# Optimization experiments

Hardware: AMD Instinct MI355X
Metric: run time of the kernel (lower is better)

## Reference

```python
import jax, jax.numpy as jnp
import numpy as np

N_QUBITS = 4
N_LAYERS = 2
DIM = 2 ** N_QUBITS  # 16
BATCH, INPUT_SIZE, HIDDEN_SIZE = 65536, 128, 512

# PennyLane default.qubit convention: wire 0 is the most significant bit.
def _cnot_perm(c, t, n=N_QUBITS):
    idx = np.arange(2 ** n)
    cbit = (idx >> (n - 1 - c)) & 1
    return np.where(cbit == 1, idx ^ (1 << (n - 1 - t)), idx)

# ring of CNOTs: control j -> target (j+1)%n
CNOT_PERMS = [jnp.asarray(_cnot_perm(j, (j + 1) % N_QUBITS)) for j in range(N_QUBITS)]
_idx = np.arange(DIM)
Z_SIGNS = jnp.asarray(np.stack([1.0 - 2.0 * ((_idx >> (N_QUBITS - 1 - j)) & 1) for j in range(N_QUBITS)], axis=1).astype(np.float32))  # [16, 4]


def _rx(t):
    c = jnp.cos(t / 2).astype(jnp.complex64)
    s = (-1j * jnp.sin(t / 2)).astype(jnp.complex64)
    return jnp.stack([jnp.stack([c, s]), jnp.stack([s, c])])


def _ry(t):
    c = jnp.cos(t / 2).astype(jnp.complex64)
    s = jnp.sin(t / 2).astype(jnp.complex64)
    return jnp.stack([jnp.stack([c, -s]), jnp.stack([s, c])])


def _rz(t):
    e = jnp.exp(-0.5j * t.astype(jnp.complex64))
    z = jnp.zeros((), jnp.complex64)
    return jnp.stack([jnp.stack([e, z]), jnp.stack([z, jnp.conj(e)])])


def _apply_1q(state, gate, j, n=N_QUBITS):
    # state: [B, 2^n] complex; gate: [2,2] (shared) or [B,2,2] (per-sample)
    B = state.shape[0]
    st = state.reshape(B, 2 ** j, 2, 2 ** (n - 1 - j))
    if gate.ndim == 2:
        st = jnp.einsum('ij,bajc->baic', gate, st)
    else:
        st = jnp.einsum('bij,bajc->baic', gate, st)
    return st.reshape(B, 2 ** n)


def _qlayer(angles, qweights):
    # Batched 4-qubit state-vector sim of the PennyLane circuit.
    # angles: [B, 4] float32 (RY embedding); qweights: [2, 4, 3]
    B = angles.shape[0]
    state = jnp.zeros((B, DIM), jnp.complex64).at[:, 0].set(1.0)
    c = jnp.cos(angles / 2).astype(jnp.complex64)
    s = jnp.sin(angles / 2).astype(jnp.complex64)
    for j in range(N_QUBITS):
        gate = jnp.stack([jnp.stack([c[:, j], -s[:, j]], -1), jnp.stack([s[:, j], c[:, j]], -1)], -2)  # [B,2,2]
        state = _apply_1q(state, gate, j)
    for l in range(N_LAYERS):
        for j in range(N_QUBITS):
            state = state[:, CNOT_PERMS[j]]
        for j in range(N_QUBITS):
            state = _apply_1q(state, _rx(qweights[l, j, 0]), j)
            state = _apply_1q(state, _ry(qweights[l, j, 1]), j)
            state = _apply_1q(state, _rz(qweights[l, j, 2]), j)
    probs = state.real ** 2 + state.imag ** 2  # [B, 16]
    return probs @ Z_SIGNS  # [B, 4] expval(PauliZ_j)


def _gate(combined, pw, pb, qw, lw, lb):
    ang = combined @ pw.T + pb  # [B, 4]
    # torch original runs the circuit on detached numpy and wraps the result in
    # torch.tensor -> no gradient flows through the quantum layer.
    q = jax.lax.stop_gradient(_qlayer(ang, qw))
    return q @ lw.T + lb  # [B, hidden]


GATES = ('forget', 'input', 'output', 'cell')


def setup_inputs() -> dict:
    key = jax.random.key(0)
    ks = jax.random.split(key, 3 + 3 * len(GATES))
    inp = {
        'x': jax.random.normal(ks[0], (BATCH, INPUT_SIZE), jnp.float32),
        'h_prev': jax.random.normal(ks[1], (BATCH, HIDDEN_SIZE), jnp.float32),
        'c_prev': jax.random.normal(ks[2], (BATCH, HIDDEN_SIZE), jnp.float32),
    }
    for i, g in enumerate(GATES):
        k0, k1, k2 = ks[3 + 3 * i], ks[4 + 3 * i], ks[5 + 3 * i]
        inp[g + '_proj_w'] = jax.random.normal(k0, (N_QUBITS, INPUT_SIZE + HIDDEN_SIZE), jnp.float32) * 0.02
        inp[g + '_proj_b'] = jnp.zeros((N_QUBITS,), jnp.float32)
        inp[g + '_qw'] = jax.random.normal(k1, (N_LAYERS, N_QUBITS, 3), jnp.float32) * 0.1
        inp[g + '_lin_w'] = jax.random.normal(k2, (HIDDEN_SIZE, N_QUBITS), jnp.float32) * 0.1
        inp[g + '_lin_b'] = jnp.zeros((HIDDEN_SIZE,), jnp.float32)
    return inp


def reference(x, h_prev, c_prev,
              forget_proj_w, forget_proj_b, forget_qw, forget_lin_w, forget_lin_b,
              input_proj_w, input_proj_b, input_qw, input_lin_w, input_lin_b,
              output_proj_w, output_proj_b, output_qw, output_lin_w, output_lin_b,
              cell_proj_w, cell_proj_b, cell_qw, cell_lin_w, cell_lin_b):
    combined = jnp.concatenate([x, h_prev], axis=1)  # [B, in+hid]
    f = jax.nn.sigmoid(_gate(combined, forget_proj_w, forget_proj_b, forget_qw, forget_lin_w, forget_lin_b))
    i = jax.nn.sigmoid(_gate(combined, input_proj_w, input_proj_b, input_qw, input_lin_w, input_lin_b))
    o = jax.nn.sigmoid(_gate(combined, output_proj_w, output_proj_b, output_qw, output_lin_w, output_lin_b))
    g = jnp.tanh(_gate(combined, cell_proj_w, cell_proj_b, cell_qw, cell_lin_w, cell_lin_b))
    c_next = f * c_prev + i * g
    h_next = o * jnp.tanh(c_next)
    return (h_next, c_next)
```

## Files before the change

### kernel.cpp

```cpp
#include <hip/hip_runtime.h>
#include <math.h>

#define BATCHN 65536
#define INPUTN 128
#define HIDDENN 512
#define CATN 640
#define ROWS_LSTM 32
#define LDSROW 144

typedef float f2v __attribute__((ext_vector_type(2)));
typedef float f4v __attribute__((ext_vector_type(4)));
typedef short s8v __attribute__((ext_vector_type(8)));

__device__ __forceinline__ unsigned short f2bf_rne(float f) {
  unsigned u = __float_as_uint(f);
  u += 0x7fffu + ((u >> 16) & 1u);
  return (unsigned short)(u >> 16);
}

__device__ __forceinline__ uint2 pack_bf16x4(float4 a) {
  uint2 u;
  asm("v_cvt_pk_bf16_f32 %0, %1, %2" : "=v"(u.x) : "v"(a.x), "v"(a.y));
  asm("v_cvt_pk_bf16_f32 %0, %1, %2" : "=v"(u.y) : "v"(a.z), "v"(a.w));
  return u;
}

__global__ void k_prologue(const float* __restrict__ qwF, const float* __restrict__ qwI,
                           const float* __restrict__ qwO, const float* __restrict__ qwC,
                           const float* __restrict__ pwF, const float* __restrict__ pwI,
                           const float* __restrict__ pwO, const float* __restrict__ pwC,
                           float2* __restrict__ U, unsigned short* __restrict__ Bfrag) {
  const int t = threadIdx.x;
  if (t < 64) {
    int g = t >> 4, col = t & 15;
    const float* qw = (g == 0) ? qwF : (g == 1) ? qwI : (g == 2) ? qwO : qwC;

    float sr[16], si[16];
#pragma unroll
    for (int i = 0; i < 16; i++) { sr[i] = (i == col) ? 1.f : 0.f; si[i] = 0.f; }

#pragma unroll
    for (int l = 0; l < 2; l++) {
#pragma unroll
      for (int j = 0; j < 4; j++) {
        const int bc = 8 >> j;
        const int bt = 8 >> ((j + 1) & 3);
        float tr[16], ti[16];
#pragma unroll
        for (int i = 0; i < 16; i++) {
          int src = (i & bc) ? (i ^ bt) : i;
          tr[i] = sr[src]; ti[i] = si[src];
        }
#pragma unroll
        for (int i = 0; i < 16; i++) { sr[i] = tr[i]; si[i] = ti[i]; }
      }
#pragma unroll
      for (int j = 0; j < 4; j++) {
        const int bit = 8 >> j;
        const float thx = qw[(l * 4 + j) * 3 + 0] * 0.5f;
        const float thy = qw[(l * 4 + j) * 3 + 1] * 0.5f;
        const float thz = qw[(l * 4 + j) * 3 + 2] * 0.5f;
        float c, s;
        c = cosf(thx); s = sinf(thx);
#pragma unroll
        for (int i = 0; i < 16; i++) if (!(i & bit)) {
          const int k2 = i | bit;
          const float ar = sr[i], ai = si[i], br = sr[k2], bi = si[k2];
          sr[i]  = c * ar + s * bi;  si[i]  = c * ai - s * br;
          sr[k2] = c * br + s * ai;  si[k2] = c * bi - s * ar;
        }
        c = cosf(thy); s = sinf(thy);
#pragma unroll
        for (int i = 0; i < 16; i++) if (!(i & bit)) {
          const int k2 = i | bit;
          const float ar = sr[i], ai = si[i], br = sr[k2], bi = si[k2];
          sr[i]  = c * ar - s * br;  si[i]  = c * ai - s * bi;
          sr[k2] = s * ar + c * br;  si[k2] = s * ai + c * bi;
        }
        c = cosf(thz); s = sinf(thz);
#pragma unroll
        for (int i = 0; i < 16; i++) if (!(i & bit)) {
          const int k2 = i | bit;
          const float ar = sr[i], ai = si[i], br = sr[k2], bi = si[k2];
          sr[i]  = c * ar + s * ai;  si[i]  = c * ai - s * ar;
          sr[k2] = c * br - s * bi;  si[k2] = c * bi + s * br;
        }
      }
    }
#pragma unroll
    for (int m = 0; m < 16; m++)
      U[(g * 16 + m) * 16 + col] = make_float2(sr[m], si[m]);
  }

  for (int e = t; e < 20 * 64; e += 256) {
    const int s = e >> 6, l = e & 63;
    const int n = l & 15, kb = l >> 4;
    const int gate = n >> 2, orow = n & 3;
    const float* pw = (gate == 0) ? pwF : (gate == 1) ? pwI : (gate == 2) ? pwO : pwC;
    const int k0 = s * 32 + kb * 8;
    unsigned short* dst = Bfrag + (size_t)e * 8;
#pragma unroll
    for (int j = 0; j < 8; ++j) dst[j] = f2bf_rne(pw[orow * CATN + k0 + j]);
  }
}

__global__ __launch_bounds__(256) void k_proj_q(
    const float* __restrict__ x, const float* __restrict__ hprev,
    const float* __restrict__ pbF, const float* __restrict__ pbI,
    const float* __restrict__ pbO, const float* __restrict__ pbC,
    const float2* __restrict__ U, const unsigned short* __restrict__ Bfrag,
    float* __restrict__ qv) {
  __shared__ char ldsA[2][64 * LDSROW];
  __shared__ float angL[64 * 17];
  const int tid = threadIdx.x;
  const int lane = tid & 63;
  const int wv = tid >> 6;
  const int m0 = wv * 16;
  const size_t rb = (size_t)blockIdx.x * 64;

  const int c4 = tid & 15;
  const int r0 = tid >> 4;

  {
    float4 v[4];
#pragma unroll
    for (int p = 0; p < 4; ++p)
      v[p] = *(const float4*)(x + (rb + r0 + p * 16) * INPUTN + c4 * 4);
#pragma unroll
    for (int p = 0; p < 4; ++p)
      *(uint2*)&ldsA[0][(r0 + p * 16) * LDSROW + c4 * 8] = pack_bf16x4(v[p]);
  }
  __syncthreads();

  f4v acc = {0.f, 0.f, 0.f, 0.f};
  const int aoff = (m0 + (lane & 15)) * LDSROW + (lane >> 4) * 16;

#pragma unroll 1
  for (int T = 0; T < 10; ++T) {
    float4 nv0, nv1, nv2, nv3;
    const bool more = (T + 1 < 10);
    if (more) {
      const int gk = (T + 1) * 64 + c4 * 4;
      const float* base = (gk < INPUTN) ? (x + gk) : (hprev + (gk - INPUTN));
      const size_t stride = (gk < INPUTN) ? INPUTN : HIDDENN;
      nv0 = *(const float4*)(base + (rb + r0 +  0) * stride);
      nv1 = *(const float4*)(base + (rb + r0 + 16) * stride);
      nv2 = *(const float4*)(base + (rb + r0 + 32) * stride);
      nv3 = *(const float4*)(base + (rb + r0 + 48) * stride);
    }
    const s8v b0 = *(const s8v*)(Bfrag + ((size_t)(T * 2 + 0) * 64 + lane) * 8);
    const s8v b1 = *(const s8v*)(Bfrag + ((size_t)(T * 2 + 1) * 64 + lane) * 8);
    const char* ab = &ldsA[T & 1][aoff];
    const s8v a0 = *(const s8v*)(ab);
    const s8v a1 = *(const s8v*)(ab + 64);
    acc = __builtin_amdgcn_mfma_f32_16x16x32_bf16(a0, b0, acc, 0, 0, 0);
    acc = __builtin_amdgcn_mfma_f32_16x16x32_bf16(a1, b1, acc, 0, 0, 0);

    if (more) {
      char* dst = ldsA[(T + 1) & 1];
      *(uint2*)&dst[(r0 +  0) * LDSROW + c4 * 8] = pack_bf16x4(nv0);
      *(uint2*)&dst[(r0 + 16) * LDSROW + c4 * 8] = pack_bf16x4(nv1);
      *(uint2*)&dst[(r0 + 32) * LDSROW + c4 * 8] = pack_bf16x4(nv2);
      *(uint2*)&dst[(r0 + 48) * LDSROW + c4 * 8] = pack_bf16x4(nv3);
      __syncthreads();
    }
  }

#pragma unroll
  for (int r = 0; r < 4; ++r)
    angL[(m0 + (lane >> 4) * 4 + r) * 17 + (lane & 15)] = acc[r];
  __syncthreads();

  const int row = tid & 63;
  const float* pbg = (wv == 0) ? pbF : (wv == 1) ? pbI : (wv == 2) ? pbO : pbC;
  float ang[4];
#pragma unroll
  for (int j = 0; j < 4; ++j) ang[j] = angL[row * 17 + wv * 4 + j] + pbg[j];

  float cs[4], sn[4];
#pragma unroll
  for (int j = 0; j < 4; j++) __sincosf(ang[j] * 0.5f, &sn[j], &cs[j]);
  float psi[16];
#pragma unroll
  for (int c16 = 0; c16 < 16; c16++) {
    float p = ((c16 & 8) ? sn[0] : cs[0]);
    p *= ((c16 & 4) ? sn[1] : cs[1]);
    p *= ((c16 & 2) ? sn[2] : cs[2]);
    p *= ((c16 & 1) ? sn[3] : cs[3]);
    psi[c16] = p;
  }
  const float2* Ug = U + wv * 256;
  float q0 = 0.f, q1 = 0.f, q2 = 0.f, q3 = 0.f;
#pragma unroll
  for (int m = 0; m < 16; m++) {
    float ssr = 0.f, ssi = 0.f;
#pragma unroll
    for (int c16 = 0; c16 < 16; c16++) {
      const float2 u = Ug[m * 16 + c16];
      ssr += u.x * psi[c16];
      ssi += u.y * psi[c16];
    }
    const float p = ssr * ssr + ssi * ssi;
    q0 = (m & 8) ? q0 - p : q0 + p;
    q1 = (m & 4) ? q1 - p : q1 + p;
    q2 = (m & 2) ? q2 - p : q2 + p;
    q3 = (m & 1) ? q3 - p : q3 + p;
  }
  *(float4*)(qv + (rb + row) * 16 + wv * 4) = make_float4(q0, q1, q2, q3);
}

__device__ __forceinline__ float sigmf(float v) {
  return __builtin_amdgcn_rcpf(1.f + __expf(-v));
}
__device__ __forceinline__ float tanhfast(float v) {
  return 1.f - 2.f * __builtin_amdgcn_rcpf(__expf(2.f * v) + 1.f);
}

__global__ __launch_bounds__(256) void k_lstm(
    const float* __restrict__ qv, const float* __restrict__ cprev,
    const float* __restrict__ lwF, const float* __restrict__ lbF,
    const float* __restrict__ lwI, const float* __restrict__ lbI,
    const float* __restrict__ lwO, const float* __restrict__ lbO,
    const float* __restrict__ lwC, const float* __restrict__ lbC,
    float* __restrict__ out) {
  const int tid = threadIdx.x;
  const int h0 = tid * 2;
  const int rb = blockIdx.x * ROWS_LSTM;

  float4 wF[2], wI[2], wO[2], wC[2];
  float bFv[2], bIv[2], bOv[2], bCv[2];
#pragma unroll
  for (int hh = 0; hh < 2; ++hh) {
    const int hp = h0 + hh;
    wF[hh] = *(const float4*)(lwF + (size_t)hp * 4);
    wI[hh] = *(const float4*)(lwI + (size_t)hp * 4);
    wO[hh] = *(const float4*)(lwO + (size_t)hp * 4);
    wC[hh] = *(const float4*)(lwC + (size_t)hp * 4);
    bFv[hh] = lbF[hp]; bIv[hh] = lbI[hp]; bOv[hh] = lbO[hp]; bCv[hh] = lbC[hp];
  }

#pragma unroll 2
  for (int it = 0; it < ROWS_LSTM; ++it) {
    const int r = rb + it;
    const float* q = qv + (size_t)r * 16;
    const float4 qF = *(const float4*)(q);
    const float4 qI = *(const float4*)(q + 4);
    const float4 qO = *(const float4*)(q + 8);
    const float4 qC = *(const float4*)(q + 12);

    const f2v cp = __builtin_nontemporal_load(
        (const f2v*)(cprev + (size_t)r * HIDDENN + h0));
    float hn[2], cn[2];
#pragma unroll
    for (int hh = 0; hh < 2; ++hh) {
      const float pf = bFv[hh] + wF[hh].x * qF.x + wF[hh].y * qF.y + wF[hh].z * qF.z + wF[hh].w * qF.w;
      const float pi = bIv[hh] + wI[hh].x * qI.x + wI[hh].y * qI.y + wI[hh].z * qI.z + wI[hh].w * qI.w;
      const float po = bOv[hh] + wO[hh].x * qO.x + wO[hh].y * qO.y + wO[hh].z * qO.z + wO[hh].w * qO.w;
      const float pg = bCv[hh] + wC[hh].x * qC.x + wC[hh].y * qC.y + wC[hh].z * qC.z + wC[hh].w * qC.w;
      const float f  = sigmf(pf);
      const float ii = sigmf(pi);
      const float oo = sigmf(po);
      const float gg = tanhfast(pg);
      const float cc = f * cp[hh] + ii * gg;
      cn[hh] = cc;
      hn[hh] = oo * tanhfast(cc);
    }
    f2v hv; hv[0] = hn[0]; hv[1] = hn[1];
    f2v cv; cv[0] = cn[0]; cv[1] = cn[1];
    __builtin_nontemporal_store(hv, (f2v*)(out + (size_t)r * HIDDENN + h0));
    __builtin_nontemporal_store(cv,
        (f2v*)(out + (size_t)BATCHN * HIDDENN + (size_t)r * HIDDENN + h0));
  }
}

extern "C" void kernel_launch(void* const* d_in, const int* in_sizes, int n_in,
                              void* d_out, int out_size, void* d_ws, size_t ws_size,
                              hipStream_t stream) {
  const float* x  = (const float*)d_in[0];
  const float* h  = (const float*)d_in[1];
  const float* c  = (const float*)d_in[2];
  const float* pwF = (const float*)d_in[3];
  const float* pbF = (const float*)d_in[4];
  const float* qwF = (const float*)d_in[5];
  const float* lwF = (const float*)d_in[6];
  const float* lbF = (const float*)d_in[7];
  const float* pwI = (const float*)d_in[8];
  const float* pbI = (const float*)d_in[9];
  const float* qwI = (const float*)d_in[10];
  const float* lwI = (const float*)d_in[11];
  const float* lbI = (const float*)d_in[12];
  const float* pwO = (const float*)d_in[13];
  const float* pbO = (const float*)d_in[14];
  const float* qwO = (const float*)d_in[15];
  const float* lwO = (const float*)d_in[16];
  const float* lbO = (const float*)d_in[17];
  const float* pwC = (const float*)d_in[18];
  const float* pbC = (const float*)d_in[19];
  const float* qwC = (const float*)d_in[20];
  const float* lwC = (const float*)d_in[21];
  const float* lbC = (const float*)d_in[22];

  float* ws = (float*)d_ws;
  float* qv = ws;
  float2* U = (float2*)(ws + (size_t)BATCHN * 16);
  unsigned short* Bfrag =
      (unsigned short*)(ws + (size_t)BATCHN * 16 + 2048);

  k_prologue<<<dim3(1), dim3(256), 0, stream>>>(qwF, qwI, qwO, qwC,
                                                pwF, pwI, pwO, pwC, U, Bfrag);
  k_proj_q<<<dim3(BATCHN / 64), dim3(256), 0, stream>>>(x, h, pbF, pbI, pbO, pbC,
                                                        U, Bfrag, qv);
  k_lstm<<<dim3(BATCHN / ROWS_LSTM), dim3(256), 0, stream>>>(qv, c, lwF, lbF, lwI, lbI,
                                                             lwO, lbO, lwC, lbC,
                                                             (float*)d_out);
}
```

Before: 139.7 us.

## Load MFMA A-operands directly from global memory, dropping LDS staging

The projection GEMM now has each lane load its A fragment straight from x and h_prev in global memory. It converts those values to bf16 in registers and feeds them to the MFMA, replacing the double-buffered LDS tile and the per-step __syncthreads. This removes the LDS writes and reads and the barrier overhead. In exchange, each lane reads two strided 32-byte chunks per row, so coalescing is worse than the previous row-contiguous float4 loads, and there is no explicit prefetch beyond unroll-2.

After: 140.2 us. About the same (+0.4%).

```diff
diff --git a/kernel.cpp b/kernel.cpp
--- a/kernel.cpp
+++ b/kernel.cpp
@@ -6,7 +6,6 @@
 #define HIDDENN 512
 #define CATN 640
 #define ROWS_LSTM 32
-#define LDSROW 144
 
 typedef float f2v __attribute__((ext_vector_type(2)));
 typedef float f4v __attribute__((ext_vector_type(4)));
@@ -18,11 +17,13 @@
   return (unsigned short)(u >> 16);
 }
 
-__device__ __forceinline__ uint2 pack_bf16x4(float4 a) {
-  uint2 u;
-  asm("v_cvt_pk_bf16_f32 %0, %1, %2" : "=v"(u.x) : "v"(a.x), "v"(a.y));
-  asm("v_cvt_pk_bf16_f32 %0, %1, %2" : "=v"(u.y) : "v"(a.z), "v"(a.w));
-  return u;
+__device__ __forceinline__ s8v pack_bf16x8(float4 lo, float4 hi) {
+  union { s8v s; unsigned u[4]; } r;
+  asm("v_cvt_pk_bf16_f32 %0, %1, %2" : "=v"(r.u[0]) : "v"(lo.x), "v"(lo.y));
+  asm("v_cvt_pk_bf16_f32 %0, %1, %2" : "=v"(r.u[1]) : "v"(lo.z), "v"(lo.w));
+  asm("v_cvt_pk_bf16_f32 %0, %1, %2" : "=v"(r.u[2]) : "v"(hi.x), "v"(hi.y));
+  asm("v_cvt_pk_bf16_f32 %0, %1, %2" : "=v"(r.u[3]) : "v"(hi.z), "v"(hi.w));
+  return r.s;
 }
 
 __global__ void k_prologue(const float* __restrict__ qwF, const float* __restrict__ qwI,
@@ -110,60 +111,41 @@
     const float* __restrict__ pbO, const float* __restrict__ pbC,
     const float2* __restrict__ U, const unsigned short* __restrict__ Bfrag,
     float* __restrict__ qv) {
-  __shared__ char ldsA[2][64 * LDSROW];
   __shared__ float angL[64 * 17];
   const int tid = threadIdx.x;
   const int lane = tid & 63;
   const int wv = tid >> 6;
   const int m0 = wv * 16;
   const size_t rb = (size_t)blockIdx.x * 64;
-
-  const int c4 = tid & 15;
-  const int r0 = tid >> 4;
-
-  {
-    float4 v[4];
-#pragma unroll
-    for (int p = 0; p < 4; ++p)
-      v[p] = *(const float4*)(x + (rb + r0 + p * 16) * INPUTN + c4 * 4);
-#pragma unroll
-    for (int p = 0; p < 4; ++p)
-      *(uint2*)&ldsA[0][(r0 + p * 16) * LDSROW + c4 * 8] = pack_bf16x4(v[p]);
-  }
-  __syncthreads();
+  const int mr = lane & 15;
+  const int kb = lane >> 4;
+  const size_t arow = rb + m0 + mr;
 
   f4v acc = {0.f, 0.f, 0.f, 0.f};
-  const int aoff = (m0 + (lane & 15)) * LDSROW + (lane >> 4) * 16;
-
-#pragma unroll 1
-  for (int T = 0; T < 10; ++T) {
-    float4 nv0, nv1, nv2, nv3;
-    const bool more = (T + 1 < 10);
-    if (more) {
-      const int gk = (T + 1) * 64 + c4 * 4;
-      const float* base = (gk < INPUTN) ? (x + gk) : (hprev + (gk - INPUTN));
-      const size_t stride = (gk < INPUTN) ? INPUTN : HIDDENN;
-      nv0 = *(const float4*)(base + (rb + r0 +  0) * stride);
-      nv1 = *(const float4*)(base + (rb + r0 + 16) * stride);
-      nv2 = *(const float4*)(base + (rb + r0 + 32) * stride);
-      nv3 = *(const float4*)(base + (rb + r0 + 48) * stride);
-    }
+
+  const float* xr = x + arow * INPUTN + kb * 8;
+#pragma unroll
+  for (int T = 0; T < 2; ++T) {
+    const float4 l0 = *(const float4*)(xr + T * 64);
+    const float4 h0 = *(const float4*)(xr + T * 64 + 4);
+    const float4 l1 = *(const float4*)(xr + T * 64 + 32);
+    const float4 h1 = *(const float4*)(xr + T * 64 + 36);
     const s8v b0 = *(const s8v*)(Bfrag + ((size_t)(T * 2 + 0) * 64 + lane) * 8);
     const s8v b1 = *(const s8v*)(Bfrag + ((size_t)(T * 2 + 1) * 64 + lane) * 8);
-    const char* ab = &ldsA[T & 1][aoff];
-    const s8v a0 = *(const s8v*)(ab);
-    const s8v a1 = *(const s8v*)(ab + 64);
-    acc = __builtin_amdgcn_mfma_f32_16x16x32_bf16(a0, b0, acc, 0, 0, 0);
-    acc = __builtin_amdgcn_mfma_f32_16x16x32_bf16(a1, b1, acc, 0, 0, 0);
-
-    if (more) {
-      char* dst = ldsA[(T + 1) & 1];
-      *(uint2*)&dst[(r0 +  0) * LDSROW + c4 * 8] = pack_bf16x4(nv0);
-      *(uint2*)&dst[(r0 + 16) * LDSROW + c4 * 8] = pack_bf16x4(nv1);
-      *(uint2*)&dst[(r0 + 32) * LDSROW + c4 * 8] = pack_bf16x4(nv2);
-      *(uint2*)&dst[(r0 + 48) * LDSROW + c4 * 8] = pack_bf16x4(nv3);
-      __syncthreads();
-    }
+    acc = __builtin_amdgcn_mfma_f32_16x16x32_bf16(pack_bf16x8(l0, h0), b0, acc, 0, 0, 0);
+    acc = __builtin_amdgcn_mfma_f32_16x16x32_bf16(pack_bf16x8(l1, h1), b1, acc, 0, 0, 0);
+  }
+  const float* hr = hprev + arow * HIDDENN + kb * 8;
+#pragma unroll 2
+  for (int T = 0; T < 8; ++T) {
+    const float4 l0 = *(const float4*)(hr + T * 64);
+    const float4 h0 = *(const float4*)(hr + T * 64 + 4);
+    const float4 l1 = *(const float4*)(hr + T * 64 + 32);
+    const float4 h1 = *(const float4*)(hr + T * 64 + 36);
+    const s8v b0 = *(const s8v*)(Bfrag + ((size_t)((T + 2) * 2 + 0) * 64 + lane) * 8);
+    const s8v b1 = *(const s8v*)(Bfrag + ((size_t)((T + 2) * 2 + 1) * 64 + lane) * 8);
+    acc = __builtin_amdgcn_mfma_f32_16x16x32_bf16(pack_bf16x8(l0, h0), b0, acc, 0, 0, 0);
+    acc = __builtin_amdgcn_mfma_f32_16x16x32_bf16(pack_bf16x8(l1, h1), b1, acc, 0, 0, 0);
   }
 
 #pragma unroll
```
